# Kernel optimization log

Hardware: AMD Instinct MI355X
Metric: run time of the kernel (lower is better)

## Reference

```python
import jax, jax.numpy as jnp
import numpy as np

SOS_TOKEN = 0
HIDDEN = 512
EMBED = 256
V_SRC = 32000
V_TGT = 50257
S_LEN = 512
T_LEN = 512


def setup_inputs() -> dict:
    key = jax.random.key(0)
    ks = jax.random.split(key, 16)
    s = 0.02
    return {
        "source": jax.random.randint(ks[0], (S_LEN,), 0, V_SRC),
        "target": jax.random.randint(ks[1], (T_LEN, 1), 0, V_TGT),
        "emb_e": jax.random.normal(ks[2], (V_SRC, EMBED), jnp.float32) * s,
        "Wih_e": jax.random.normal(ks[3], (3 * HIDDEN, EMBED), jnp.float32) * s,
        "Whh_e": jax.random.normal(ks[4], (3 * HIDDEN, HIDDEN), jnp.float32) * s,
        "bih_e": jax.random.normal(ks[5], (3 * HIDDEN,), jnp.float32) * s,
        "bhh_e": jax.random.normal(ks[6], (3 * HIDDEN,), jnp.float32) * s,
        "emb_d": jax.random.normal(ks[7], (V_TGT, EMBED), jnp.float32) * s,
        "Wih_d": jax.random.normal(ks[8], (3 * HIDDEN, EMBED), jnp.float32) * s,
        "Whh_d": jax.random.normal(ks[9], (3 * HIDDEN, HIDDEN), jnp.float32) * s,
        "bih_d": jax.random.normal(ks[10], (3 * HIDDEN,), jnp.float32) * s,
        "bhh_d": jax.random.normal(ks[11], (3 * HIDDEN,), jnp.float32) * s,
        "Wout": jax.random.normal(ks[12], (V_TGT, HIDDEN), jnp.float32) * s,
        "bout": jax.random.normal(ks[13], (V_TGT,), jnp.float32) * s,
    }


def _gru_step(h, x, Wih, Whh, bih, bhh):
    # PyTorch GRU cell: gates ordered (r, z, n)
    gi = Wih @ x + bih            # [3H]
    gh = Whh @ h + bhh            # [3H]
    gi_r, gi_z, gi_n = jnp.split(gi, 3)
    gh_r, gh_z, gh_n = jnp.split(gh, 3)
    r = jax.nn.sigmoid(gi_r + gh_r)
    z = jax.nn.sigmoid(gi_z + gh_z)
    n = jnp.tanh(gi_n + r * gh_n)
    return (1.0 - z) * n + z * h


def reference(source, target, emb_e, Wih_e, Whh_e, bih_e, bhh_e,
              emb_d, Wih_d, Whh_d, bih_d, bhh_d, Wout, bout):
    # Encoder (faithful to original: gru called per-token with zero hidden,
    # so only the last source token determines encoder_hidden).
    x_last = emb_e[source[-1]]                       # [E]
    h0 = jnp.zeros((HIDDEN,), dtype=emb_e.dtype)
    h_enc = _gru_step(h0, x_last, Wih_e, Whh_e, bih_e, bhh_e)  # [H]

    # Decoder with teacher forcing (ratio=1.0): inputs are SOS, target[:-1]
    tgt = target[:, 0]
    tokens = jnp.concatenate([jnp.array([SOS_TOKEN], dtype=tgt.dtype), tgt[:-1]])

    def step(h, tok):
        x = jax.nn.relu(emb_d[tok])                  # [E]
        h2 = _gru_step(h, x, Wih_d, Whh_d, bih_d, bhh_d)
        logp = jax.nn.log_softmax(Wout @ h2 + bout)  # [V]
        return h2, logp

    _, logps = jax.lax.scan(step, h_enc, tokens)     # [T, V]
    return logps[:, None, :]                         # [T, 1, V]
```

## Files before the change

### kernel.cpp

```cpp
#include <hip/hip_runtime.h>
#include <stdint.h>

#define HIDDEN 512
#define EMBED  256
#define VTGT   50257
#define TLEN   512
#define GATE3  1536
#define REC_B  16
#define GEMM_B 224
#define NBLK   (REC_B + GEMM_B)
#define NJT    ((VTGT + 127) / 128)

typedef float f32x4 __attribute__((ext_vector_type(4)));
typedef unsigned int u32;
typedef unsigned int u32x4 __attribute__((ext_vector_type(4)));

__device__ __forceinline__ unsigned short f2bf(float f) {
  union { float f; unsigned u; } v; v.f = f;
  unsigned u = v.u;
  unsigned r = (u + 0x7FFFu + ((u >> 16) & 1u)) >> 16;
  return (unsigned short)r;
}

__device__ __forceinline__ float sigm(float x) {
  return __builtin_amdgcn_rcpf(1.f + __expf(-x));
}
__device__ __forceinline__ float fast_tanh(float x) {
  return 1.f - 2.f * __builtin_amdgcn_rcpf(__expf(2.f * x) + 1.f);
}

__device__ __forceinline__ u32 cpoll(const u32* p) {
  u32 v;
  asm volatile("global_load_dword %0, %1, off sc0 sc1\n\ts_waitcnt vmcnt(0)"
               : "=v"(v) : "v"(p) : "memory");
  return v;
}
__device__ __forceinline__ void cload4x4(const u32* p, u32x4& a, u32x4& b,
                                         u32x4& c, u32x4& d) {
  asm volatile(
      "global_load_dwordx4 %0, %4, off sc0 sc1\n\t"
      "global_load_dwordx4 %1, %4, off offset:16 sc0 sc1\n\t"
      "global_load_dwordx4 %2, %4, off offset:32 sc0 sc1\n\t"
      "global_load_dwordx4 %3, %4, off offset:48 sc0 sc1\n\t"
      "s_waitcnt vmcnt(0)"
      : "=v"(a), "=v"(b), "=v"(c), "=v"(d) : "v"(p) : "memory");
}
__device__ __forceinline__ void cload2(const u32* p0, const u32* p1,
                                       u32x4& a, u32x4& b) {
  asm volatile(
      "global_load_dwordx4 %0, %2, off sc0 sc1\n\t"
      "global_load_dwordx4 %1, %3, off sc0 sc1\n\t"
      "s_waitcnt vmcnt(0)"
      : "=v"(a), "=v"(b) : "v"(p0), "v"(p1) : "memory");
}
__device__ __forceinline__ void cstore(u32* p, u32 v) {
  asm volatile("global_store_dword %0, %1, off sc0 sc1" :: "v"(p), "v"(v) : "memory");
}
__device__ __forceinline__ void cstore4(u32* p, u32x4 v) {
  asm volatile("global_store_dwordx4 %0, %1, off sc0 sc1" :: "v"(p), "v"(v) : "memory");
}

__global__ void kenc1(const int* source, const float* emb_e, const float* Wih_e,
                      const float* bih_e, float* genc) {
  __shared__ float xs[EMBED];
  int tid = threadIdx.x;
  int tok = source[511];
  if (tid < EMBED) xs[tid] = emb_e[(size_t)tok * EMBED + tid];
  __syncthreads();
  int j = blockIdx.x * 256 + tid;
  const float* w = Wih_e + (size_t)j * EMBED;
  float acc = bih_e[j];
  for (int k = 0; k < EMBED; k += 4) {
    float4 wv = *(const float4*)(w + k);
    acc += wv.x * xs[k] + wv.y * xs[k + 1] + wv.z * xs[k + 2] + wv.w * xs[k + 3];
  }
  genc[j] = acc;
}

__global__ void kenc2(const float* genc, const float* bhh_e, u32* hs) {
  int e = threadIdx.x;
  float r = sigm(genc[e] + bhh_e[e]);
  float z = sigm(genc[e + 512] + bhh_e[e + 512]);
  float n = tanhf(genc[e + 1024] + r * bhh_e[e + 1024]);
  float h = (1.f - z) * n;
  hs[e] = (__float_as_uint(h) & ~511u) | 256u;
}

__global__ __launch_bounds__(256) void kgi(const int* target, const float* emb_d,
                                           const float* Wih_d, const float* bih_d,
                                           float* GI) {
  __shared__ float Xs[32][EMBED];
  int tid = threadIdx.x;
  int j0 = blockIdx.x * 128;
  int t0 = blockIdx.y * 32;
  for (int idx = tid; idx < 32 * EMBED; idx += 256) {
    int tt = idx >> 8, c = idx & 255;
    int t = t0 + tt;
    int tok = (t == 0) ? 0 : target[t - 1];
    float v = emb_d[(size_t)tok * EMBED + c];
    Xs[tt][c] = v > 0.f ? v : 0.f;
  }
  __syncthreads();
  int jl = tid & 127, tg = tid >> 7;
  int j = j0 + jl;
  const float* w = Wih_d + (size_t)j * EMBED;
  float acc[16];
#pragma unroll
  for (int i = 0; i < 16; ++i) acc[i] = 0.f;
  for (int k = 0; k < EMBED; k += 4) {
    float4 wv = *(const float4*)(w + k);
#pragma unroll
    for (int i = 0; i < 16; ++i) {
      int tl = tg * 16 + i;
      acc[i] += wv.x * Xs[tl][k] + wv.y * Xs[tl][k + 1] +
                wv.z * Xs[tl][k + 2] + wv.w * Xs[tl][k + 3];
    }
  }
  float b = bih_d[j];
#pragma unroll
  for (int i = 0; i < 16; ++i) {
    int t = t0 + tg * 16 + i;
    GI[(size_t)t * GATE3 + j] = acc[i] + b;
  }
}

#define DOT4(w, h) (w[0]*h[0] + w[1]*h[1] + w[2]*h[2] + w[3]*h[3])

__device__ void rec_path(int bid, const float* __restrict__ Whh,
                         const float* __restrict__ bhh,
                         const float* __restrict__ GI, u32* hs, u32* stepv,
                         char* SM) {
  int tid = threadIdx.x;
  int p = tid & 15, r = tid >> 4;
  int e = bid * 32 + r;
  int k0 = p * 32;
  float* hbuf = (float*)SM;
  const f32x4* Wr = (const f32x4*)(Whh + (size_t)e * HIDDEN + k0);
  const f32x4* Wz = (const f32x4*)(Whh + (size_t)(e + 512) * HIDDEN + k0);
  const f32x4* Wn = (const f32x4*)(Whh + (size_t)(e + 1024) * HIDDEN + k0);
  f32x4 wr0 = Wr[0], wr1 = Wr[1], wr2 = Wr[2], wr3 = Wr[3],
        wr4 = Wr[4], wr5 = Wr[5], wr6 = Wr[6], wr7 = Wr[7];
  f32x4 wz0 = Wz[0], wz1 = Wz[1], wz2 = Wz[2], wz3 = Wz[3],
        wz4 = Wz[4], wz5 = Wz[5], wz6 = Wz[6], wz7 = Wz[7];
  f32x4 wn0 = Wn[0], wn1 = Wn[1], wn2 = Wn[2], wn3 = Wn[3],
        wn4 = Wn[4], wn5 = Wn[5], wn6 = Wn[6], wn7 = Wn[7];
  float br = bhh[e], bz = bhh[e + 512], bn = bhh[e + 1024];
  float hold = __uint_as_float(hs[e] & ~511u);
  __builtin_amdgcn_s_setprio(1);
  int lane = tid & 63;
  int d0 = lane * 4;
  int i0 = ((d0 >> 5) * 36) + (d0 & 31);
  int i1 = (((d0 + 256) >> 5) * 36) + (d0 & 31);
  int w = tid >> 6;
  u32* pubbase = hs + bid * 32 + w * 4;
  for (int t = 0; t < TLEN; ++t) {
    int par = t & 1;
    float gie = 0.f, giz = 0.f, gin = 0.f;
    if (p == 0) {
      const float* git = GI + (size_t)t * GATE3;
      gie = git[e]; giz = git[e + 512]; gin = git[e + 1024];
    }
    if (tid < 128) {
      const u32* s0 = hs + (size_t)t * HIDDEN + d0;
      const u32* s1 = s0 + 256;
      u32 want = 256u + ((u32)t & 255u);
      u32x4 a, b;
      for (;;) {
        cload2(s0, s1, a, b);
        u32 bad = 0;
#pragma unroll
        for (int q = 0; q < 4; ++q) bad |= (a[q] ^ want) | (b[q] ^ want);
        if (!__any((bad & 511u) != 0u)) break;
      }
      f32x4 fa, fb;
#pragma unroll
      for (int q = 0; q < 4; ++q) {
        fa[q] = __uint_as_float(a[q] & ~511u);
        fb[q] = __uint_as_float(b[q] & ~511u);
      }
      *(f32x4*)&hbuf[par * 576 + i0] = fa;
      *(f32x4*)&hbuf[par * 576 + i1] = fb;
    }
    __syncthreads();
    if (bid == 0 && tid == 0) cstore(stepv, (u32)t);
    const f32x4* hp4 = (const f32x4*)(hbuf + par * 576 + p * 36);
    f32x4 h0 = hp4[0], h1 = hp4[1], h2 = hp4[2], h3 = hp4[3],
          h4 = hp4[4], h5 = hp4[5], h6 = hp4[6], h7 = hp4[7];
    float pr = DOT4(wr0, h0) + DOT4(wr1, h1) + DOT4(wr2, h2) + DOT4(wr3, h3) +
               DOT4(wr4, h4) + DOT4(wr5, h5) + DOT4(wr6, h6) + DOT4(wr7, h7);
    float pz = DOT4(wz0, h0) + DOT4(wz1, h1) + DOT4(wz2, h2) + DOT4(wz3, h3) +
               DOT4(wz4, h4) + DOT4(wz5, h5) + DOT4(wz6, h6) + DOT4(wz7, h7);
    float pn = DOT4(wn0, h0) + DOT4(wn1, h1) + DOT4(wn2, h2) + DOT4(wn3, h3) +
               DOT4(wn4, h4) + DOT4(wn5, h5) + DOT4(wn6, h6) + DOT4(wn7, h7);
#pragma unroll
    for (int m = 1; m < 16; m <<= 1) {
      pr += __shfl_xor(pr, m);
      pz += __shfl_xor(pz, m);
      pn += __shfl_xor(pn, m);
    }
    u32 pk = 0;
    if (p == 0) {
      float rg = sigm(gie + pr + br);
      float z  = sigm(giz + pz + bz);
      float n  = fast_tanh(gin + rg * (pn + bn));
      float hnew = (1.f - z) * n + z * hold;
      hold = hnew;
      pk = (__float_as_uint(hnew) & ~511u) | (256u + ((u32)(t + 1) & 255u));
    }
    u32x4 o;
    o[0] = __shfl(pk, 0);  o[1] = __shfl(pk, 16);
    o[2] = __shfl(pk, 32); o[3] = __shfl(pk, 48);
    if ((tid & 63) == 0) cstore4(pubbase + (size_t)(t + 1) * HIDDEN, o);
  }
  if (bid == 0 && tid < 64) {
    const u32* s0 = hs + (size_t)TLEN * HIDDEN + d0;
    const u32* s1 = s0 + 256;
    u32 want = 256u + ((u32)TLEN & 255u);
    u32x4 a, b;
    for (;;) {
      cload2(s0, s1, a, b);
      u32 bad = 0;
#pragma unroll
      for (int q = 0; q < 4; ++q) bad |= (a[q] ^ want) | (b[q] ^ want);
      if (!__any((bad & 511u) != 0u)) break;
    }
    if (tid == 0) cstore(stepv, (u32)TLEN);
  }
}

__device__ void gemm_path(int g, const u32* hs, u32* stepv, const float* Wout,
                          const float* bout, float* rs, float* out, char* SM) {
  unsigned short* As = (unsigned short*)SM;
  float* rsum = (float*)(SM + 64 * 520 * 2);
  int tid = threadIdx.x;
  int w = tid >> 6, lane = tid & 63;
  int jl = lane & 15, kq = lane >> 4;
  int srow = tid >> 3, scg = tid & 7;
  if (tid < 64) rsum[tid] = 0.f;
  for (int t0i = 0; t0i < 8; ++t0i) {
    int t0 = t0i * 64;
    if (tid == 0) {
      while ((int)cpoll(stepv) < t0 + 64) __builtin_amdgcn_s_sleep(16);
    }
    __syncthreads();
    int slot = t0 + srow + 1;
    u32 want = 256u + ((u32)slot & 255u);
    const u32* sbase = hs + (size_t)slot * HIDDEN + scg * 64;
#pragma unroll
    for (int b = 0; b < 4; ++b) {
      const u32* sp = sbase + b * 16;
      u32x4 c0, c1, c2, c3;
      for (;;) {
        cload4x4(sp, c0, c1, c2, c3);
        u32 bad = 0;
#pragma unroll
        for (int q = 0; q < 4; ++q)
          bad |= (c0[q] ^ want) | (c1[q] ^ want) | (c2[q] ^ want) | (c3[q] ^ want);
        if (!(bad & 511u)) break;
      }
      u32 dw[8];
#pragma unroll
      for (int q = 0; q < 4; ++q) {
        u32x4 cq = (q == 0) ? c0 : (q == 1) ? c1 : (q == 2) ? c2 : c3;
        float f0 = __uint_as_float(cq[0] & ~511u);
        float f1 = __uint_as_float(cq[1] & ~511u);
        float f2 = __uint_as_float(cq[2] & ~511u);
        float f3 = __uint_as_float(cq[3] & ~511u);
        dw[q * 2]     = (u32)f2bf(f0) | ((u32)f2bf(f1) << 16);
        dw[q * 2 + 1] = (u32)f2bf(f2) | ((u32)f2bf(f3) << 16);
      }
      *(u32x4*)&As[srow * 520 + scg * 64 + b * 16]     = *(u32x4*)&dw[0];
      *(u32x4*)&As[srow * 520 + scg * 64 + b * 16 + 8] = *(u32x4*)&dw[4];
    }
    __syncthreads();
    for (int jt = g; jt < NJT; jt += GEMM_B) {
      int j = jt * 128 + w * 16 + jl;
      int jc = j < VTGT ? j : VTGT - 1;
      const float* Bp = Wout + (size_t)jc * HIDDEN + kq * 8;
      f32x4 acc[4];
#pragma unroll
      for (int i = 0; i < 4; ++i) acc[i] = (f32x4)(0.f);
#pragma unroll
      for (int ks = 0; ks < 16; ++ks) {
        float4 b0 = *(const float4*)(Bp + ks * 32);
        float4 b1 = *(const float4*)(Bp + ks * 32 + 4);
        u32x4 bf;
        bf[0] = (u32)f2bf(b0.x) | ((u32)f2bf(b0.y) << 16);
        bf[1] = (u32)f2bf(b0.z) | ((u32)f2bf(b0.w) << 16);
        bf[2] = (u32)f2bf(b1.x) | ((u32)f2bf(b1.y) << 16);
        bf[3] = (u32)f2bf(b1.z) | ((u32)f2bf(b1.w) << 16);
#pragma unroll
        for (int tq = 0; tq < 4; ++tq) {
          u32x4 af = *(const u32x4*)&As[(tq * 16 + jl) * 520 + ks * 32 + kq * 8];
          asm volatile("v_mfma_f32_16x16x32_bf16 %0, %1, %2, %0"
                       : "+v"(acc[tq]) : "v"(af), "v"(bf));
        }
      }
      asm volatile("s_nop 7\n\ts_nop 7\n\ts_nop 7" ::);
      bool jok = j < VTGT;
      float bj = jok ? bout[j] : 0.f;
#pragma unroll
      for (int tq = 0; tq < 4; ++tq) {
#pragma unroll
        for (int rr = 0; rr < 4; ++rr) {
          int t = t0 + tq * 16 + kq * 4 + rr;
          float lg = acc[tq][rr] + bj;
          if (jok) out[(size_t)t * VTGT + j] = lg;
          float ex = jok ? __expf(lg) : 0.f;
#pragma unroll
          for (int m = 1; m < 16; m <<= 1) ex += __shfl_xor(ex, m);
          if (jl == 0) atomicAdd(&rsum[tq * 16 + kq * 4 + rr], ex);
        }
      }
    }
    __syncthreads();
    if (tid < 64) {
      atomicAdd(rs + t0 + tid, rsum[tid]);
      rsum[tid] = 0.f;
    }
  }
}

__global__ __launch_bounds__(512, 2) void kmain(const float* Whh, const float* bhh,
                                                const float* GI, u32* hs, u32* stepv,
                                                const float* Wout, const float* bout,
                                                float* rs, float* out) {
  __shared__ __align__(16) char SM[64 * 520 * 2 + 256];
  int bid = blockIdx.x;
  if (bid < REC_B) rec_path(bid, Whh, bhh, GI, hs, stepv, SM);
  else gemm_path(bid - REC_B, hs, stepv, Wout, bout, rs, out, SM);
}

__global__ __launch_bounds__(1024) void klsub(float* out, const float* rs) {
  int t = blockIdx.x;
  float l = logf(rs[t]);
  float* row = out + (size_t)t * VTGT;
  for (int jj = threadIdx.x; jj < VTGT; jj += 1024) row[jj] -= l;
}

extern "C" void kernel_launch(void* const* d_in, const int* in_sizes, int n_in,
                              void* d_out, int out_size, void* d_ws, size_t ws_size,
                              hipStream_t stream) {
  const int*   source = (const int*)d_in[0];
  const int*   target = (const int*)d_in[1];
  const float* emb_e  = (const float*)d_in[2];
  const float* Wih_e  = (const float*)d_in[3];
  const float* bih_e  = (const float*)d_in[5];
  const float* bhh_e  = (const float*)d_in[6];
  const float* emb_d  = (const float*)d_in[7];
  const float* Wih_d  = (const float*)d_in[8];
  const float* Whh_d  = (const float*)d_in[9];
  const float* bih_d  = (const float*)d_in[10];
  const float* bhh_d  = (const float*)d_in[11];
  const float* Wout   = (const float*)d_in[12];
  const float* bout   = (const float*)d_in[13];
  float* out = (float*)d_out;
  char* ws = (char*)d_ws;

  float* GI    = (float*)(ws + 0);
  u32*   hs    = (u32*)(ws + 3145728);
  u32*   stepv = (u32*)(ws + 4196352);
  float* rs    = (float*)(ws + 4196480);
  float* genc  = (float*)(ws + 4198528);

  hipMemsetAsync(hs, 0, 1052800, stream);
  kenc1<<<6, 256, 0, stream>>>(source, emb_e, Wih_e, bih_e, genc);
  kenc2<<<1, 512, 0, stream>>>(genc, bhh_e, hs);
  kgi<<<dim3(12, 16), 256, 0, stream>>>(target, emb_d, Wih_d, bih_d, GI);
  kmain<<<NBLK, 512, 0, stream>>>(Whh_d, bhh_d, GI, hs, stepv, Wout, bout, rs, out);
  klsub<<<512, 1024, 0, stream>>>(out, rs);
}
```

Baseline: 897.2 us.

## Co-locate recurrent blocks on one XCC and sync hidden state via L2-scoped flags

Blocks now pick their role at runtime. Each reads its XCC id, counts per-XCC arrivals with atomics, and the 16 recurrent roles go to blocks on a single XCC. The recurrent blocks then exchange hidden state through a buffer written and polled with sc0-only (L2-coherent) stores and loads, which avoids system-scope round trips. A mirrored copy is also written with full coherence for the GEMM blocks on other XCCs, plus a bounded-retry fallback to that mirror. The cost is extra stores, a grid-wide arrival barrier at launch, and a dependence on all blocks being co-resident.

```diff
diff --git a/kernel.cpp b/kernel.cpp
--- a/kernel.cpp
+++ b/kernel.cpp
@@ -58,6 +58,17 @@
 }
 __device__ __forceinline__ void cstore4(u32* p, u32x4 v) {
   asm volatile("global_store_dwordx4 %0, %1, off sc0 sc1" :: "v"(p), "v"(v) : "memory");
+}
+__device__ __forceinline__ void cload2_l(const u32* p0, const u32* p1,
+                                         u32x4& a, u32x4& b) {
+  asm volatile(
+      "global_load_dwordx4 %0, %2, off sc0\n\t"
+      "global_load_dwordx4 %1, %3, off sc0\n\t"
+      "s_waitcnt vmcnt(0)"
+      : "=v"(a), "=v"(b) : "v"(p0), "v"(p1) : "memory");
+}
+__device__ __forceinline__ void cstore4_l(u32* p, u32x4 v) {
+  asm volatile("global_store_dwordx4 %0, %1, off sc0" :: "v"(p), "v"(v) : "memory");
 }
 
 __global__ void kenc1(const int* source, const float* emb_e, const float* Wih_e,
@@ -77,13 +88,15 @@
   genc[j] = acc;
 }
 
-__global__ void kenc2(const float* genc, const float* bhh_e, u32* hs) {
+__global__ void kenc2(const float* genc, const float* bhh_e, u32* hs, u32* hsm) {
   int e = threadIdx.x;
   float r = sigm(genc[e] + bhh_e[e]);
   float z = sigm(genc[e + 512] + bhh_e[e + 512]);
   float n = tanhf(genc[e + 1024] + r * bhh_e[e + 1024]);
   float h = (1.f - z) * n;
-  hs[e] = (__float_as_uint(h) & ~511u) | 256u;
+  u32 pk = (__float_as_uint(h) & ~511u) | 256u;
+  hs[e] = pk;
+  hsm[e] = pk;
 }
 
 __global__ __launch_bounds__(256) void kgi(const int* target, const float* emb_d,
@@ -126,13 +139,13 @@
 
 #define DOT4(w, h) (w[0]*h[0] + w[1]*h[1] + w[2]*h[2] + w[3]*h[3])
 
-__device__ void rec_path(int bid, const float* __restrict__ Whh,
+__device__ void rec_path(int slot, const float* __restrict__ Whh,
                          const float* __restrict__ bhh,
-                         const float* __restrict__ GI, u32* hs, u32* stepv,
-                         char* SM) {
+                         const float* __restrict__ GI, u32* hs, u32* hsm,
+                         u32* stepv, char* SM) {
   int tid = threadIdx.x;
   int p = tid & 15, r = tid >> 4;
-  int e = bid * 32 + r;
+  int e = slot * 32 + r;
   int k0 = p * 32;
   float* hbuf = (float*)SM;
   const f32x4* Wr = (const f32x4*)(Whh + (size_t)e * HIDDEN + k0);
@@ -152,7 +165,9 @@
   int i0 = ((d0 >> 5) * 36) + (d0 & 31);
   int i1 = (((d0 + 256) >> 5) * 36) + (d0 & 31);
   int w = tid >> 6;
-  u32* pubbase = hs + bid * 32 + w * 4;
+  u32* pub_l = hs + slot * 32 + w * 4;
+  u32* pub_m = hsm + slot * 32 + w * 4;
+  int fb = 0;
   for (int t = 0; t < TLEN; ++t) {
     int par = t & 1;
     float gie = 0.f, giz = 0.f, gin = 0.f;
@@ -165,24 +180,38 @@
       const u32* s1 = s0 + 256;
       u32 want = 256u + ((u32)t & 255u);
       u32x4 a, b;
-      for (;;) {
-        cload2(s0, s1, a, b);
+      bool ok = false;
+      int tries = (fb >= 8) ? 0 : 24;
+      for (int it = 0; it < tries && !ok; ++it) {
+        cload2_l(s0, s1, a, b);
         u32 bad = 0;
 #pragma unroll
         for (int q = 0; q < 4; ++q) bad |= (a[q] ^ want) | (b[q] ^ want);
-        if (!__any((bad & 511u) != 0u)) break;
-      }
-      f32x4 fa, fb;
+        ok = !__any((bad & 511u) != 0u);
+      }
+      if (!ok) {
+        ++fb;
+        const u32* m0 = hsm + (size_t)t * HIDDEN + d0;
+        const u32* m1 = m0 + 256;
+        do {
+          cload2(m0, m1, a, b);
+          u32 bad = 0;
+#pragma unroll
+          for (int q = 0; q < 4; ++q) bad |= (a[q] ^ want) | (b[q] ^ want);
+          ok = !__any((bad & 511u) != 0u);
+        } while (!ok);
+      }
+      f32x4 fa, fc;
 #pragma unroll
       for (int q = 0; q < 4; ++q) {
         fa[q] = __uint_as_float(a[q] & ~511u);
-        fb[q] = __uint_as_float(b[q] & ~511u);
+        fc[q] = __uint_as_float(b[q] & ~511u);
       }
       *(f32x4*)&hbuf[par * 576 + i0] = fa;
-      *(f32x4*)&hbuf[par * 576 + i1] = fb;
+      *(f32x4*)&hbuf[par * 576 + i1] = fc;
     }
     __syncthreads();
-    if (bid == 0 && tid == 0) cstore(stepv, (u32)t);
+    if (slot == 0 && tid == 128) cstore(stepv, (u32)t);
     const f32x4* hp4 = (const f32x4*)(hbuf + par * 576 + p * 36);
     f32x4 h0 = hp4[0], h1 = hp4[1], h2 = hp4[2], h3 = hp4[3],
           h4 = hp4[4], h5 = hp4[5], h6 = hp4[6], h7 = hp4[7];
@@ -210,15 +239,18 @@
     u32x4 o;
     o[0] = __shfl(pk, 0);  o[1] = __shfl(pk, 16);
     o[2] = __shfl(pk, 32); o[3] = __shfl(pk, 48);
-    if ((tid & 63) == 0) cstore4(pubbase + (size_t)(t + 1) * HIDDEN, o);
-  }
-  if (bid == 0 && tid < 64) {
-    const u32* s0 = hs + (size_t)TLEN * HIDDEN + d0;
-    const u32* s1 = s0 + 256;
+    if ((tid & 63) == 0) {
+      cstore4_l(pub_l + (size_t)(t + 1) * HIDDEN, o);
+      cstore4(pub_m + (size_t)(t + 1) * HIDDEN, o);
+    }
+  }
+  if (slot == 0 && tid < 64) {
+    const u32* m0 = hsm + (size_t)TLEN * HIDDEN + d0;
+    const u32* m1 = m0 + 256;
     u32 want = 256u + ((u32)TLEN & 255u);
     u32x4 a, b;
     for (;;) {
-      cload2(s0, s1, a, b);
+      cload2(m0, m1, a, b);
       u32 bad = 0;
 #pragma unroll
       for (int q = 0; q < 4; ++q) bad |= (a[q] ^ want) | (b[q] ^ want);
@@ -228,7 +260,7 @@
   }
 }
 
-__device__ void gemm_path(int g, const u32* hs, u32* stepv, const float* Wout,
+__device__ void gemm_path(int g, const u32* hsm, u32* stepv, const float* Wout,
                           const float* bout, float* rs, float* out, char* SM) {
   unsigned short* As = (unsigned short*)SM;
   float* rsum = (float*)(SM + 64 * 520 * 2);
@@ -245,7 +277,7 @@
     __syncthreads();
     int slot = t0 + srow + 1;
     u32 want = 256u + ((u32)slot & 255u);
-    const u32* sbase = hs + (size_t)slot * HIDDEN + scg * 64;
+    const u32* sbase = hsm + (size_t)slot * HIDDEN + scg * 64;
 #pragma unroll
     for (int b = 0; b < 4; ++b) {
       const u32* sp = sbase + b * 16;
@@ -322,13 +354,39 @@
 }
 
 __global__ __launch_bounds__(512, 2) void kmain(const float* Whh, const float* bhh,
-                                                const float* GI, u32* hs, u32* stepv,
+                                                const float* GI, u32* hs, u32* hsm,
+                                                u32* stepv, u32* ctl,
                                                 const float* Wout, const float* bout,
                                                 float* rs, float* out) {
   __shared__ __align__(16) char SM[64 * 520 * 2 + 256];
-  int bid = blockIdx.x;
-  if (bid < REC_B) rec_path(bid, Whh, bhh, GI, hs, stepv, SM);
-  else gemm_path(bid - REC_B, hs, stepv, Wout, bout, rs, out, SM);
+  __shared__ int role;
+  int tid = threadIdx.x;
+  if (tid == 0) {
+    u32 xcc;
+    asm volatile("s_getreg_b32 %0, hwreg(HW_REG_XCC_ID)" : "=s"(xcc));
+    xcc &= 7u;
+    u32 myt = __hip_atomic_fetch_add(&ctl[xcc], 1u, __ATOMIC_RELAXED,
+                                     __HIP_MEMORY_SCOPE_AGENT);
+    __hip_atomic_fetch_add(&ctl[8], 1u, __ATOMIC_RELEASE, __HIP_MEMORY_SCOPE_AGENT);
+    while (__hip_atomic_load(&ctl[8], __ATOMIC_ACQUIRE, __HIP_MEMORY_SCOPE_AGENT)
+           < (u32)NBLK)
+      __builtin_amdgcn_s_sleep(8);
+    int rx = 0;
+    for (int x = 0; x < 8; ++x) {
+      u32 c = __hip_atomic_load(&ctl[x], __ATOMIC_RELAXED, __HIP_MEMORY_SCOPE_AGENT);
+      if (c >= (u32)REC_B) { rx = x; break; }
+    }
+    if ((int)xcc == rx && myt < (u32)REC_B) {
+      role = (int)myt;
+    } else {
+      role = -1 - (int)__hip_atomic_fetch_add(&ctl[9], 1u, __ATOMIC_RELAXED,
+                                              __HIP_MEMORY_SCOPE_AGENT);
+    }
+  }
+  __syncthreads();
+  int rl = role;
+  if (rl >= 0) rec_path(rl, Whh, bhh, GI, hs, hsm, stepv, SM);
+  else gemm_path(-1 - rl, hsm, stepv, Wout, bout, rs, out, SM);
 }
 
 __global__ __launch_bounds__(1024) void klsub(float* out, const float* rs) {
@@ -359,14 +417,17 @@
 
   float* GI    = (float*)(ws + 0);
   u32*   hs    = (u32*)(ws + 3145728);
-  u32*   stepv = (u32*)(ws + 4196352);
-  float* rs    = (float*)(ws + 4196480);
-  float* genc  = (float*)(ws + 4198528);
-
-  hipMemsetAsync(hs, 0, 1052800, stream);
+  u32*   hsm   = (u32*)(ws + 4196352);
+  u32*   stepv = (u32*)(ws + 5246976);
+  float* rs    = (float*)(ws + 5247104);
+  u32*   ctl   = (u32*)(ws + 5249152);
+  float* genc  = (float*)(ws + 5249280);
+
+  hipMemsetAsync(ws + 3145728, 0, 2103552, stream);
   kenc1<<<6, 256, 0, stream>>>(source, emb_e, Wih_e, bih_e, genc);
-  kenc2<<<1, 512, 0, stream>>>(genc, bhh_e, hs);
+  kenc2<<<1, 512, 0, stream>>>(genc, bhh_e, hs, hsm);
   kgi<<<dim3(12, 16), 256, 0, stream>>>(target, emb_d, Wih_d, bih_d, GI);
-  kmain<<<NBLK, 512, 0, stream>>>(Whh_d, bhh_d, GI, hs, stepv, Wout, bout, rs, out);
+  kmain<<<NBLK, 512, 0, stream>>>(Whh_d, bhh_d, GI, hs, hsm, stepv, ctl,
+                                  Wout, bout, rs, out);
   klsub<<<512, 1024, 0, stream>>>(out, rs);
 }
```

Measured after the change: 859.6 us. 1.04x faster.
